# Optimization experiments

Measured on AMD Instinct MI355X. Metric: run time of the kernel, lower is better.

## Reference

```python
import jax, jax.numpy as jnp
import numpy as np


def _lstm_layer(xs, Wih, Whh, bih, bhh):
    # xs: [B, T, D_in]; PyTorch gate order: i, f, g, o
    B = xs.shape[0]
    H = Whh.shape[1]
    b = bih + bhh

    def step(carry, xt):
        h, c = carry
        g = xt @ Wih.T + h @ Whh.T + b          # [B, 4H]
        i, f, gg, o = jnp.split(g, 4, axis=-1)
        c = jax.nn.sigmoid(f) * c + jax.nn.sigmoid(i) * jnp.tanh(gg)
        h = jax.nn.sigmoid(o) * jnp.tanh(c)
        return (h, c), h

    h0 = jnp.zeros((B, H), xs.dtype)
    _, hs = jax.lax.scan(step, (h0, h0), xs.transpose(1, 0, 2))
    return hs.transpose(1, 0, 2)                # [B, T, H]


def setup_inputs() -> dict:
    key = jax.random.key(0)
    B, T, K, H, OUT = 64, 512, 8, 256, 24       # K = input_size = n fc heads
    HID1, HID2 = 100, 128                       # SAGE hidden / out feats

    ks = jax.random.split(key, 24)

    def rn(k, shape, s=0.05):
        return jax.random.normal(k, shape, dtype=jnp.float32) * s

    return {
        "x": jax.random.normal(ks[0], (B, T, K), dtype=jnp.float32),
        # LSTM layer 0
        "Wih0": rn(ks[1], (4 * H, K)), "Whh0": rn(ks[2], (4 * H, H)),
        "bih0": rn(ks[3], (4 * H,)),   "bhh0": rn(ks[4], (4 * H,)),
        # LSTM layer 1
        "Wih1": rn(ks[5], (4 * H, H)), "Whh1": rn(ks[6], (4 * H, H)),
        "bih1": rn(ks[7], (4 * H,)),   "bhh1": rn(ks[8], (4 * H,)),
        # SAGEConv1: lin_l (aggregated, with bias) + lin_r (root)
        "Wl1": rn(ks[9], (HID1, H)), "Wr1": rn(ks[10], (HID1, H)), "b1": rn(ks[11], (HID1,)),
        # SAGEConv2
        "Wl2": rn(ks[12], (HID2, HID1)), "Wr2": rn(ks[13], (HID2, HID1)), "b2": rn(ks[14], (HID2,)),
        # K stacked fc heads: Linear(128,64) -> ReLU -> Linear(64,OUT)
        "Wfc1": rn(ks[15], (K, 64, HID2)), "bfc1": rn(ks[16], (K, 64)),
        "Wfc2": rn(ks[17], (K, OUT, 64)),  "bfc2": rn(ks[18], (K, OUT)),
    }


def reference(x, Wih0, Whh0, bih0, bhh0, Wih1, Whh1, bih1, bhh1,
              Wl1, Wr1, b1, Wl2, Wr2, b2, Wfc1, bfc1, Wfc2, bfc2):
    # 2-layer LSTM (eval mode, dropout inactive)
    h = _lstm_layer(x, Wih0, Whh0, bih0, bhh0)   # [B, T, H]
    h = _lstm_layer(h, Wih1, Whh1, bih1, bhh1)   # [B, T, H]

    # softmax(feat@feat.T) > 0 everywhere => complete graph incl. self-loops,
    # and edge_weight is unused by GraphSAGE.forward, so SAGEConv mean aggregation
    # reduces exactly to the mean over all T nodes per graph.
    m = h.mean(axis=1, keepdims=True)            # [B, 1, H]
    h1 = jax.nn.elu(m @ Wl1.T + b1 + h @ Wr1.T)  # [B, T, 100]
    m1 = h1.mean(axis=1, keepdims=True)
    h2 = m1 @ Wl2.T + b2 + h1 @ Wr2.T            # [B, T, 128]

    s = h2[:, -1, :]                             # [B, 128] (last node)

    z = jax.nn.relu(jnp.einsum('bd,kod->kbo', s, Wfc1) + bfc1[:, None, :])
    pred = jnp.einsum('kbo,kpo->kbp', z, Wfc2) + bfc2[:, None, :]
    return pred                                   # [K, B, output_size]
```

## Files before the change

### kernel.cpp

```cpp
#include <hip/hip_runtime.h>
#include <stdint.h>

typedef _Float16 f16;
typedef _Float16 h2 __attribute__((ext_vector_type(2)));
typedef float f4 __attribute__((ext_vector_type(4)));

union F4H { f4 v; h2 h[4]; f16 s[8]; };

__device__ __forceinline__ float fdot2(h2 a, h2 b, float c) {
    return __builtin_amdgcn_fdot2(a, b, c, false);
}

__device__ __forceinline__ void lbar() {
    __builtin_amdgcn_sched_barrier(0);
    asm volatile("s_waitcnt lgkmcnt(0)" ::: "memory");
    __builtin_amdgcn_s_barrier();
    __builtin_amdgcn_sched_barrier(0);
}

#define NB 64
#define NT 512
#define NH 256
#define NG 1024

static const size_t OFF_H0   = 0;
static const size_t OFF_X1   = 16777216;
static const size_t OFF_H1   = 83886080;
static const size_t OFF_PL0  = 100663296;
static const size_t OFF_PL1  = 101187584;
static const size_t OFF_WIH1 = 101711872;
static const size_t OFF_WX0  = 102236160;
static const size_t OFF_B0C  = 102252544;
static const size_t OFF_B1C  = 102256640;
static const size_t OFF_WR1  = 102260736;
static const size_t OFF_MM   = 102326272;
static const size_t OFF_M1S  = 102391808;
static const size_t OFF_HL   = 102424576;
static const size_t OFF_FLG  = OFF_HL;

__device__ __forceinline__ void packw(const float* src, f4* dst, int id)
{
    const int j = id >> 5;
    const int g = id & 31;
    const float* s = src + j * 256 + g * 8;
    F4H u;
    #pragma unroll
    for (int i = 0; i < 8; ++i) u.s[i] = (f16)s[i];
    dst[g * 1024 + j] = u.v;
}

__global__ void pack_all(const float* __restrict__ Whh0, const float* __restrict__ Whh1,
                         const float* __restrict__ Wih1, const float* __restrict__ wih0,
                         const float* __restrict__ bih0, const float* __restrict__ bhh0,
                         const float* __restrict__ bih1, const float* __restrict__ bhh1,
                         const float* __restrict__ wr1,
                         f4* __restrict__ pl0, f4* __restrict__ pl1, f4* __restrict__ wih1p,
                         float* __restrict__ b0c, float* __restrict__ b1c,
                         h2* __restrict__ wx0p, f4* __restrict__ wr1p)
{
    const int id = blockIdx.x * 256 + threadIdx.x;
    if (id < 32768) {
        packw(Whh0, pl0, id);
    } else if (id < 65536) {
        packw(Whh1, pl1, id - 32768);
    } else if (id < 98304) {
        packw(Wih1, wih1p, id - 65536);
    } else if (id < 99328) {
        const int j = id - 98304;
        b0c[j] = bih0[j] + bhh0[j];
    } else if (id < 100352) {
        const int j = id - 99328;
        b1c[j] = bih1[j] + bhh1[j];
    } else if (id < 104448) {
        const int q = id - 100352;
        const int p = q >> 10, j = q & 1023;
        h2 v; v[0] = (f16)wih0[j * 8 + 2 * p]; v[1] = (f16)wih0[j * 8 + 2 * p + 1];
        wx0p[p * 1024 + j] = v;
    } else {
        const int q = id - 104448;
        const int g = q >> 7, o = q & 127;
        F4H u;
        #pragma unroll
        for (int i = 0; i < 8; ++i)
            u.s[i] = (o < 100) ? (f16)wr1[o * 256 + g * 8 + i] : (f16)0.f;
        wr1p[g * 128 + o] = u.v;
    }
}

#define DOT8(wa_, wb_, hh_) { F4H wa_u; wa_u.v = (wa_); F4H wb_u; wb_u.v = (wb_); F4H hh_u; hh_u.v = (hh_); \
    a0  = fdot2(wa_u.h[0], hh_u.h[0], a0 ); a1  = fdot2(wb_u.h[0], hh_u.h[0], a1 ); \
    a0b = fdot2(wa_u.h[1], hh_u.h[1], a0b); a1b = fdot2(wb_u.h[1], hh_u.h[1], a1b); \
    a0  = fdot2(wa_u.h[2], hh_u.h[2], a0 ); a1  = fdot2(wb_u.h[2], hh_u.h[2], a1 ); \
    a0b = fdot2(wa_u.h[3], hh_u.h[3], a0b); a1b = fdot2(wb_u.h[3], hh_u.h[3], a1b); }

#define STREAM_PHASES(HV) \
    _Pragma("unroll") \
    for (int p = 0; p < 6; ++p) { \
        if ((p & 1) == 0) { \
            DOT8(pA0[0], pA1[0], (HV)[20 + 2 * p]); \
            DOT8(pA0[1], pA1[1], (HV)[21 + 2 * p]); \
            if (p < 4) { \
                pA0[0] = str[(2 * (p + 2))     * 1024 + j0]; \
                pA1[0] = str[(2 * (p + 2))     * 1024 + j1]; \
                pA0[1] = str[(2 * (p + 2) + 1) * 1024 + j0]; \
                pA1[1] = str[(2 * (p + 2) + 1) * 1024 + j1]; \
            } \
        } else { \
            DOT8(pB0[0], pB1[0], (HV)[20 + 2 * p]); \
            DOT8(pB0[1], pB1[1], (HV)[21 + 2 * p]); \
            if (p < 4) { \
                pB0[0] = str[(2 * (p + 2))     * 1024 + j0]; \
                pB1[0] = str[(2 * (p + 2))     * 1024 + j1]; \
                pB0[1] = str[(2 * (p + 2) + 1) * 1024 + j0]; \
                pB1[1] = str[(2 * (p + 2) + 1) * 1024 + j1]; \
            } \
        } \
        DOT8(wrA[2 * p], wrB[2 * p], (HV)[9 + 2 * p]); \
        if (p < 5) DOT8(wrA[2 * p + 1], wrB[2 * p + 1], (HV)[10 + 2 * p]); \
    }

__global__ __launch_bounds__(512, 2)
void mega(const float* __restrict__ x,
          const f4* __restrict__ pl0, const f4* __restrict__ pl1,
          const f4* __restrict__ wih1p,
          const float* __restrict__ b0c, const float* __restrict__ b1c,
          const h2* __restrict__ wx0p,
          f16* __restrict__ h0, f16* __restrict__ x1, f16* __restrict__ h1,
          float* __restrict__ mmean, unsigned int* __restrict__ flags)
{
    __shared__ f4 wlds[9 * 1024];
    __shared__ float gates[1024];
    __shared__ __align__(16) f16 hsh[256];
    __shared__ __align__(16) h2 xsh[512 * 4];

    const int t = threadIdx.x;
    const int bid = blockIdx.x;
    const int role = bid >> 6;
    const int b = bid & 63;
    const int j0 = t, j1 = t + 512;

    if (role == 0) {
        const f4* pack = pl0;
        #pragma unroll
        for (int i = 0; i < 18; ++i) wlds[t + 512 * i] = pack[t + 512 * i];
        f4 wrA[11], wrB[11];
        #pragma unroll
        for (int g = 0; g < 11; ++g) {
            wrA[g] = pack[(9 + g) * 1024 + j0];
            wrB[g] = pack[(9 + g) * 1024 + j1];
        }
        #pragma unroll
        for (int g = 0; g < 11; ++g)
            asm volatile("" : "+v"(wrA[g]), "+v"(wrB[g]));
        const f4* str = pack + 20 * 1024;

        const float bc0 = b0c[j0], bc1 = b0c[j1];
        h2 wxA[4], wxB[4];
        #pragma unroll
        for (int p = 0; p < 4; ++p) { wxA[p] = wx0p[p * 1024 + j0]; wxB[p] = wx0p[p * 1024 + j1]; }
        const float* xb = x + ((size_t)b * NT + t) * 8;
        #pragma unroll
        for (int p = 0; p < 4; ++p) {
            h2 v; v[0] = (f16)xb[2 * p]; v[1] = (f16)xb[2 * p + 1];
            xsh[t * 4 + p] = v;
        }
        if (t < 32) { f4 zz = {0.f, 0.f, 0.f, 0.f}; ((f4*)hsh)[t] = zz; }
        float cst = 0.f;
        __syncthreads();

        f16* houtb = h0 + (size_t)b * NT * NH;
        unsigned int* myfl = flags + b * 16;

        #pragma unroll 1
        for (int tt = 0; tt < NT; ++tt) {
            f4 pA0[2], pA1[2], pB0[2], pB1[2];
            #pragma unroll
            for (int g = 0; g < 2; ++g) { pA0[g] = str[g * 1024 + j0]; pA1[g] = str[g * 1024 + j1]; }
            float a0 = bc0, a1 = bc1, a0b = 0.f, a1b = 0.f;
            #pragma unroll
            for (int p = 0; p < 4; ++p) {
                h2 xv = xsh[tt * 4 + p];
                a0 = fdot2(wxA[p], xv, a0);
                a1 = fdot2(wxB[p], xv, a1);
            }
            #pragma unroll
            for (int g = 0; g < 2; ++g) { pB0[g] = str[(2 + g) * 1024 + j0]; pB1[g] = str[(2 + g) * 1024 + j1]; }

            const f4* hv4 = (const f4*)hsh;
            #pragma unroll
            for (int i = 0; i < 9; ++i) DOT8(wlds[i * 1024 + j0], wlds[i * 1024 + j1], hv4[i]);
            STREAM_PHASES(hv4)

            gates[j0] = a0 + a0b;
            gates[j1] = a1 + a1b;
            lbar();

            if (t < 256) {
                float gi = gates[t], gf = gates[t + 256], gg = gates[t + 512], go = gates[t + 768];
                float si = 1.f / (1.f + __expf(-gi));
                float sf = 1.f / (1.f + __expf(-gf));
                float so = 1.f / (1.f + __expf(-go));
                float tg = 1.f - 2.f / (__expf(2.f * gg) + 1.f);
                cst = sf * cst + si * tg;
                float th = 1.f - 2.f / (__expf(2.f * cst) + 1.f);
                float hvl = so * th;
                hsh[t] = (f16)hvl;
                houtb[(size_t)tt * NH + t] = (f16)hvl;
            }
            if (((tt + 1) & 15) == 0) {
                __syncthreads();
                if (t == 0)
                    __hip_atomic_store(myfl, (unsigned)(tt + 1),
                                       __ATOMIC_RELEASE, __HIP_MEMORY_SCOPE_AGENT);
            } else {
                lbar();
            }
        }
    } else if (role == 1) {
        const float bc0 = b1c[j0], bc1 = b1c[j1];
        const f16* h0b = h0 + (size_t)b * NT * NH;
        f16* x1b = x1 + (size_t)b * NT * NG;
        const unsigned int* pfl = flags + b * 16;
        unsigned int* myfl = flags + 1024 + b * 16;
        f16* hrows = (f16*)xsh;
        bool dead = false;

        #pragma unroll 1
        for (int c = 0; c < 32; ++c) {
            if (t < 64 && !dead) {
                unsigned int guard = 0;
                while (__hip_atomic_load(pfl, __ATOMIC_ACQUIRE, __HIP_MEMORY_SCOPE_AGENT)
                       < (unsigned)((c + 1) * 16)) {
                    __builtin_amdgcn_s_sleep(8);
                    if (++guard > (1u << 16)) { dead = true; break; }
                }
            }
            __syncthreads();
            {
                const int rr = t >> 5, cc = t & 31;
                ((f4*)hrows)[t] = ((const f4*)(h0b + (size_t)(c * 16 + rr) * NH))[cc];
            }
            __syncthreads();

            float acc0[16], acc1[16];
            #pragma unroll
            for (int r = 0; r < 16; ++r) { acc0[r] = bc0; acc1[r] = bc1; }

            f4 w0 = wih1p[j0], w1 = wih1p[j1];
            #pragma unroll 1
            for (int g = 0; g < 32; ++g) {
                f4 n0 = w0, n1 = w1;
                if (g < 31) { n0 = wih1p[(g + 1) * 1024 + j0]; n1 = wih1p[(g + 1) * 1024 + j1]; }
                F4H W0; W0.v = w0; F4H W1; W1.v = w1;
                #pragma unroll
                for (int r = 0; r < 16; ++r) {
                    F4H H; H.v = ((const f4*)hrows)[r * 32 + g];
                    acc0[r] = fdot2(W0.h[0], H.h[0], acc0[r]);
                    acc0[r] = fdot2(W0.h[1], H.h[1], acc0[r]);
                    acc0[r] = fdot2(W0.h[2], H.h[2], acc0[r]);
                    acc0[r] = fdot2(W0.h[3], H.h[3], acc0[r]);
                    acc1[r] = fdot2(W1.h[0], H.h[0], acc1[r]);
                    acc1[r] = fdot2(W1.h[1], H.h[1], acc1[r]);
                    acc1[r] = fdot2(W1.h[2], H.h[2], acc1[r]);
                    acc1[r] = fdot2(W1.h[3], H.h[3], acc1[r]);
                }
                w0 = n0; w1 = n1;
            }
            #pragma unroll
            for (int r = 0; r < 16; ++r) {
                x1b[(size_t)(c * 16 + r) * NG + j0] = (f16)acc0[r];
                x1b[(size_t)(c * 16 + r) * NG + j1] = (f16)acc1[r];
            }
            __syncthreads();
            if (t == 0) __hip_atomic_store(myfl, (unsigned)(c + 1),
                                           __ATOMIC_RELEASE, __HIP_MEMORY_SCOPE_AGENT);
        }
    } else {
        const f4* pack = pl1;
        #pragma unroll
        for (int i = 0; i < 18; ++i) wlds[t + 512 * i] = pack[t + 512 * i];
        f4 wrA[11], wrB[11];
        #pragma unroll
        for (int g = 0; g < 11; ++g) {
            wrA[g] = pack[(9 + g) * 1024 + j0];
            wrB[g] = pack[(9 + g) * 1024 + j1];
        }
        #pragma unroll
        for (int g = 0; g < 11; ++g)
            asm volatile("" : "+v"(wrA[g]), "+v"(wrB[g]));
        const f4* str = pack + 20 * 1024;

        if (t < 32) { f4 zz = {0.f, 0.f, 0.f, 0.f}; ((f4*)hsh)[t] = zz; }
        float cst = 0.f, hsum = 0.f;
        __syncthreads();
        const f16* x1b = x1 + (size_t)b * NT * NG;
        f16* houtb = h1 + (size_t)b * NT * NH;
        const unsigned int* pfl = flags + 1024 + b * 16;
        bool dead = false;

        #pragma unroll 1
        for (int tt = 0; tt < NT; ++tt) {
            if ((tt & 15) == 0) {
                if (t < 64 && !dead) {
                    unsigned int guard = 0;
                    while (__hip_atomic_load(pfl, __ATOMIC_ACQUIRE, __HIP_MEMORY_SCOPE_AGENT)
                           < (unsigned)((tt >> 4) + 1)) {
                        __builtin_amdgcn_s_sleep(8);
                        if (++guard > (1u << 16)) { dead = true; break; }
                    }
                }
                __syncthreads();
            }

            f4 pA0[2], pA1[2], pB0[2], pB1[2];
            #pragma unroll
            for (int g = 0; g < 2; ++g) { pA0[g] = str[g * 1024 + j0]; pA1[g] = str[g * 1024 + j1]; }
            #pragma unroll
            for (int g = 0; g < 2; ++g) { pB0[g] = str[(2 + g) * 1024 + j0]; pB1[g] = str[(2 + g) * 1024 + j1]; }

            const f16* xr = x1b + (size_t)tt * NG;
            float a0 = (float)xr[j0];
            float a1 = (float)xr[j1];
            float a0b = 0.f, a1b = 0.f;

            const f4* hv4 = (const f4*)hsh;
            #pragma unroll
            for (int i = 0; i < 9; ++i) DOT8(wlds[i * 1024 + j0], wlds[i * 1024 + j1], hv4[i]);
            STREAM_PHASES(hv4)

            gates[j0] = a0 + a0b;
            gates[j1] = a1 + a1b;
            lbar();

            if (t < 256) {
                float gi = gates[t], gf = gates[t + 256], gg = gates[t + 512], go = gates[t + 768];
                float si = 1.f / (1.f + __expf(-gi));
                float sf = 1.f / (1.f + __expf(-gf));
                float so = 1.f / (1.f + __expf(-go));
                float tg = 1.f - 2.f / (__expf(2.f * gg) + 1.f);
                cst = sf * cst + si * tg;
                float th = 1.f - 2.f / (__expf(2.f * cst) + 1.f);
                float hvl = so * th;
                hsh[t] = (f16)hvl;
                houtb[(size_t)tt * NH + t] = (f16)hvl;
                hsum += hvl;
            }
            lbar();
        }
        if (t < 256) mmean[b * NH + t] = hsum * (1.f / 512.f);
    }
}

__global__ __launch_bounds__(256)
void k4a(const f16* __restrict__ h1, const float* __restrict__ mmean,
         const float* __restrict__ Wl1, const float* __restrict__ b1,
         const f4* __restrict__ wr1p, float* __restrict__ m1sum,
         float* __restrict__ hh1last)
{
    __shared__ __align__(16) f16 ash[64 * 256];
    __shared__ float msh[256];
    __shared__ float mbase[128];
    __shared__ float red[256];
    const int l = threadIdx.x;
    const int b = blockIdx.x >> 3;
    const int ch = blockIdx.x & 7;

    const f4* src = (const f4*)(h1 + ((size_t)b * 512 + ch * 64) * 256);
    f4* dst = (f4*)ash;
    #pragma unroll
    for (int i = 0; i < 8; ++i) dst[l + 256 * i] = src[l + 256 * i];
    msh[l] = mmean[b * 256 + l];
    __syncthreads();

    if (l < 128) {
        float acc = 0.f;
        if (l < 100) {
            acc = b1[l];
            const float* wrow = Wl1 + l * 256;
            for (int j = 0; j < 256; ++j) acc += msh[j] * wrow[j];
        }
        mbase[l] = acc;
    }
    __syncthreads();

    const int o = l & 127;
    const int th = l >> 7;
    float sumloc = 0.f;
    float last = 0.f;
    #pragma unroll 1
    for (int it = 0; it < 32; ++it) {
        const int tloc = it * 2 + th;
        float acc = mbase[o];
        const f4* arow = (const f4*)(ash + tloc * 256);
        #pragma unroll
        for (int u = 0; u < 32; ++u) {
            F4H av; av.v = arow[u];
            F4H wv; wv.v = wr1p[u * 128 + o];
            #pragma unroll
            for (int p = 0; p < 4; ++p) acc = fdot2(av.h[p], wv.h[p], acc);
        }
        float e = acc > 0.f ? acc : (__expf(acc) - 1.f);
        sumloc += e;
        if (tloc == 63) last = e;
    }
    red[l] = sumloc;
    __syncthreads();
    if (l < 128) {
        float s = red[l] + red[l + 128];
        if (l < 100) atomicAdd(m1sum + b * 128 + l, s);
    }
    if (ch == 7 && th == 1) hh1last[b * 128 + o] = last;
}

__global__ __launch_bounds__(128)
void k4b(const float* __restrict__ m1sum, const float* __restrict__ hh1last,
         const float* __restrict__ Wl2, const float* __restrict__ Wr2,
         const float* __restrict__ b2,
         const float* __restrict__ Wfc1, const float* __restrict__ bfc1,
         const float* __restrict__ Wfc2, const float* __restrict__ bfc2,
         float* __restrict__ out)
{
    __shared__ float m1s[128];
    __shared__ float hl[128];
    __shared__ float s[128];
    __shared__ float zsh[512];
    const int b = blockIdx.x;
    const int l = threadIdx.x;

    m1s[l] = m1sum[b * 128 + l] * (1.f / 512.f);
    hl[l] = hh1last[b * 128 + l];
    __syncthreads();

    {
        float acc = b2[l];
        const float* wl2r = Wl2 + l * 100;
        const float* wr2r = Wr2 + l * 100;
        for (int j = 0; j < 100; ++j) acc += m1s[j] * wl2r[j] + hl[j] * wr2r[j];
        s[l] = acc;
    }
    __syncthreads();

    #pragma unroll 1
    for (int i = 0; i < 4; ++i) {
        const int idx = l + 128 * i;
        const int k = idx >> 6, o = idx & 63;
        const float* w = Wfc1 + (size_t)(k * 64 + o) * 128;
        float a = bfc1[k * 64 + o];
        for (int d = 0; d < 128; ++d) a += s[d] * w[d];
        zsh[idx] = a > 0.f ? a : 0.f;
    }
    __syncthreads();

    #pragma unroll 1
    for (int i = 0; i < 2; ++i) {
        const int idx = l + 128 * i;
        if (idx < 192) {
            const int k = idx / 24, p = idx % 24;
            const float* w = Wfc2 + (size_t)(k * 24 + p) * 64;
            float a = bfc2[k * 24 + p];
            const float* z = zsh + k * 64;
            for (int d = 0; d < 64; ++d) a += z[d] * w[d];
            out[(size_t)(k * 64 + b) * 24 + p] = a;
        }
    }
}

extern "C" void kernel_launch(void* const* d_in, const int* in_sizes, int n_in,
                              void* d_out, int out_size, void* d_ws, size_t ws_size,
                              hipStream_t stream)
{
    const float* x    = (const float*)d_in[0];
    const float* Wih0 = (const float*)d_in[1];
    const float* Whh0 = (const float*)d_in[2];
    const float* bih0 = (const float*)d_in[3];
    const float* bhh0 = (const float*)d_in[4];
    const float* Wih1 = (const float*)d_in[5];
    const float* Whh1 = (const float*)d_in[6];
    const float* bih1 = (const float*)d_in[7];
    const float* bhh1 = (const float*)d_in[8];
    const float* Wl1  = (const float*)d_in[9];
    const float* Wr1  = (const float*)d_in[10];
    const float* b1   = (const float*)d_in[11];
    const float* Wl2  = (const float*)d_in[12];
    const float* Wr2  = (const float*)d_in[13];
    const float* b2   = (const float*)d_in[14];
    const float* Wfc1 = (const float*)d_in[15];
    const float* bfc1 = (const float*)d_in[16];
    const float* Wfc2 = (const float*)d_in[17];
    const float* bfc2 = (const float*)d_in[18];

    char* ws = (char*)d_ws;
    f16*   h0f   = (f16*)(ws + OFF_H0);
    f16*   x1f   = (f16*)(ws + OFF_X1);
    f16*   h1f   = (f16*)(ws + OFF_H1);
    f4*    pl0   = (f4*)(ws + OFF_PL0);
    f4*    pl1   = (f4*)(ws + OFF_PL1);
    f4*    wih1p = (f4*)(ws + OFF_WIH1);
    h2*    wx0p  = (h2*)(ws + OFF_WX0);
    float* b0c   = (float*)(ws + OFF_B0C);
    float* b1c   = (float*)(ws + OFF_B1C);
    f4*    wr1p  = (f4*)(ws + OFF_WR1);
    float* mm    = (float*)(ws + OFF_MM);
    float* m1s   = (float*)(ws + OFF_M1S);
    float* hhl   = (float*)(ws + OFF_HL);
    unsigned int* flg = (unsigned int*)(ws + OFF_FLG);

    pack_all<<<424, 256, 0, stream>>>(Whh0, Whh1, Wih1, Wih0,
                                      bih0, bhh0, bih1, bhh1, Wr1,
                                      pl0, pl1, wih1p, b0c, b1c, wx0p, wr1p);
    hipMemsetAsync(m1s, 0, 64 * 128 * sizeof(float), stream);
    hipMemsetAsync(flg, 0, 8192, stream);

    mega<<<192, 512, 0, stream>>>(x, pl0, pl1, wih1p, b0c, b1c, wx0p,
                                  h0f, x1f, h1f, mm, flg);

    k4a<<<512, 256, 0, stream>>>(h1f, mm, Wl1, b1, wr1p, m1s, hhl);
    k4b<<<64, 128, 0, stream>>>(m1s, hhl, Wl2, Wr2, b2, Wfc1, bfc1, Wfc2, bfc2, (float*)d_out);
}
```

Measured before the change: 1.256 ms.

## Permute gate columns so lane pairs hold all four gates, drop LDS gate exchange

The packed weights and biases are permuted so that each thread pair (t, t^1) computes the i,f,g,o gates for the same hidden unit. The gate pre-activations are then exchanged with a lane shuffle instead of being written to shared memory. This removes one block barrier per timestep, and the hidden state is double-buffered so the remaining barrier suffices. The cost is that every thread now evaluates the activation math, half of it redundantly, and the layout change depends on the pairing matching the pack order exactly.

```diff
diff --git a/kernel.cpp b/kernel.cpp
--- a/kernel.cpp
+++ b/kernel.cpp
@@ -38,11 +38,17 @@
 static const size_t OFF_HL   = 102424576;
 static const size_t OFF_FLG  = OFF_HL;
 
+__device__ __forceinline__ int permcol(int slot) {
+    const int s = slot & 511;
+    const int u = s >> 1, c = s & 1;
+    return (slot >> 9) * 512 + u + c * 256;
+}
+
 __device__ __forceinline__ void packw(const float* src, f4* dst, int id)
 {
     const int j = id >> 5;
     const int g = id & 31;
-    const float* s = src + j * 256 + g * 8;
+    const float* s = src + permcol(j) * 256 + g * 8;
     F4H u;
     #pragma unroll
     for (int i = 0; i < 8; ++i) u.s[i] = (f16)s[i];
@@ -67,14 +73,17 @@
         packw(Wih1, wih1p, id - 65536);
     } else if (id < 99328) {
         const int j = id - 98304;
-        b0c[j] = bih0[j] + bhh0[j];
+        const int pc = permcol(j);
+        b0c[j] = bih0[pc] + bhh0[pc];
     } else if (id < 100352) {
         const int j = id - 99328;
-        b1c[j] = bih1[j] + bhh1[j];
+        const int pc = permcol(j);
+        b1c[j] = bih1[pc] + bhh1[pc];
     } else if (id < 104448) {
         const int q = id - 100352;
         const int p = q >> 10, j = q & 1023;
-        h2 v; v[0] = (f16)wih0[j * 8 + 2 * p]; v[1] = (f16)wih0[j * 8 + 2 * p + 1];
+        const int pc = permcol(j);
+        h2 v; v[0] = (f16)wih0[pc * 8 + 2 * p]; v[1] = (f16)wih0[pc * 8 + 2 * p + 1];
         wx0p[p * 1024 + j] = v;
     } else {
         const int q = id - 104448;
@@ -129,8 +138,7 @@
           float* __restrict__ mmean, unsigned int* __restrict__ flags)
 {
     __shared__ f4 wlds[9 * 1024];
-    __shared__ float gates[1024];
-    __shared__ __align__(16) f16 hsh[256];
+    __shared__ __align__(16) f16 hbuf[2][256];
     __shared__ __align__(16) h2 xsh[512 * 4];
 
     const int t = threadIdx.x;
@@ -164,12 +172,13 @@
             h2 v; v[0] = (f16)xb[2 * p]; v[1] = (f16)xb[2 * p + 1];
             xsh[t * 4 + p] = v;
         }
-        if (t < 32) { f4 zz = {0.f, 0.f, 0.f, 0.f}; ((f4*)hsh)[t] = zz; }
+        if (t < 32) { f4 zz = {0.f, 0.f, 0.f, 0.f}; ((f4*)hbuf)[t] = zz; }
         float cst = 0.f;
         __syncthreads();
 
         f16* houtb = h0 + (size_t)b * NT * NH;
         unsigned int* myfl = flags + b * 16;
+        const int u = t >> 1, odd = t & 1;
 
         #pragma unroll 1
         for (int tt = 0; tt < NT; ++tt) {
@@ -186,26 +195,29 @@
             #pragma unroll
             for (int g = 0; g < 2; ++g) { pB0[g] = str[(2 + g) * 1024 + j0]; pB1[g] = str[(2 + g) * 1024 + j1]; }
 
-            const f4* hv4 = (const f4*)hsh;
+            const f4* hv4 = ((const f4*)hbuf) + (tt & 1) * 32;
             #pragma unroll
             for (int i = 0; i < 9; ++i) DOT8(wlds[i * 1024 + j0], wlds[i * 1024 + j1], hv4[i]);
             STREAM_PHASES(hv4)
 
-            gates[j0] = a0 + a0b;
-            gates[j1] = a1 + a1b;
-            lbar();
-
-            if (t < 256) {
-                float gi = gates[t], gf = gates[t + 256], gg = gates[t + 512], go = gates[t + 768];
-                float si = 1.f / (1.f + __expf(-gi));
-                float sf = 1.f / (1.f + __expf(-gf));
-                float so = 1.f / (1.f + __expf(-go));
-                float tg = 1.f - 2.f / (__expf(2.f * gg) + 1.f);
-                cst = sf * cst + si * tg;
-                float th = 1.f - 2.f / (__expf(2.f * cst) + 1.f);
-                float hvl = so * th;
-                hsh[t] = (f16)hvl;
-                houtb[(size_t)tt * NH + t] = (f16)hvl;
+            float av = a0 + a0b;
+            float bv = a1 + a1b;
+            float fa = __shfl_xor(av, 1, 64);
+            float fb = __shfl_xor(bv, 1, 64);
+            float gi = odd ? fa : av;
+            float gf = odd ? av : fa;
+            float gg = odd ? fb : bv;
+            float go = odd ? bv : fb;
+            float si = 1.f / (1.f + __expf(-gi));
+            float sf = 1.f / (1.f + __expf(-gf));
+            float so = 1.f / (1.f + __expf(-go));
+            float tg = 1.f - 2.f / (__expf(2.f * gg) + 1.f);
+            cst = sf * cst + si * tg;
+            float th = 1.f - 2.f / (__expf(2.f * cst) + 1.f);
+            float hvl = so * th;
+            if (!odd) {
+                hbuf[(tt & 1) ^ 1][u] = (f16)hvl;
+                houtb[(size_t)tt * NH + u] = (f16)hvl;
             }
             if (((tt + 1) & 15) == 0) {
                 __syncthreads();
@@ -290,13 +302,14 @@
             asm volatile("" : "+v"(wrA[g]), "+v"(wrB[g]));
         const f4* str = pack + 20 * 1024;
 
-        if (t < 32) { f4 zz = {0.f, 0.f, 0.f, 0.f}; ((f4*)hsh)[t] = zz; }
+        if (t < 32) { f4 zz = {0.f, 0.f, 0.f, 0.f}; ((f4*)hbuf)[t] = zz; }
         float cst = 0.f, hsum = 0.f;
         __syncthreads();
         const f16* x1b = x1 + (size_t)b * NT * NG;
         f16* houtb = h1 + (size_t)b * NT * NH;
         const unsigned int* pfl = flags + 1024 + b * 16;
         bool dead = false;
+        const int u = t >> 1, odd = t & 1;
 
         #pragma unroll 1
         for (int tt = 0; tt < NT; ++tt) {
@@ -323,31 +336,34 @@
             float a1 = (float)xr[j1];
             float a0b = 0.f, a1b = 0.f;
 
-            const f4* hv4 = (const f4*)hsh;
+            const f4* hv4 = ((const f4*)hbuf) + (tt & 1) * 32;
             #pragma unroll
             for (int i = 0; i < 9; ++i) DOT8(wlds[i * 1024 + j0], wlds[i * 1024 + j1], hv4[i]);
             STREAM_PHASES(hv4)
 
-            gates[j0] = a0 + a0b;
-            gates[j1] = a1 + a1b;
+            float av = a0 + a0b;
+            float bv = a1 + a1b;
+            float fa = __shfl_xor(av, 1, 64);
+            float fb = __shfl_xor(bv, 1, 64);
+            float gi = odd ? fa : av;
+            float gf = odd ? av : fa;
+            float gg = odd ? fb : bv;
+            float go = odd ? bv : fb;
+            float si = 1.f / (1.f + __expf(-gi));
+            float sf = 1.f / (1.f + __expf(-gf));
+            float so = 1.f / (1.f + __expf(-go));
+            float tg = 1.f - 2.f / (__expf(2.f * gg) + 1.f);
+            cst = sf * cst + si * tg;
+            float th = 1.f - 2.f / (__expf(2.f * cst) + 1.f);
+            float hvl = so * th;
+            if (!odd) {
+                hbuf[(tt & 1) ^ 1][u] = (f16)hvl;
+                houtb[(size_t)tt * NH + u] = (f16)hvl;
+                hsum += hvl;
+            }
             lbar();
-
-            if (t < 256) {
-                float gi = gates[t], gf = gates[t + 256], gg = gates[t + 512], go = gates[t + 768];
-                float si = 1.f / (1.f + __expf(-gi));
-                float sf = 1.f / (1.f + __expf(-gf));
-                float so = 1.f / (1.f + __expf(-go));
-                float tg = 1.f - 2.f / (__expf(2.f * gg) + 1.f);
-                cst = sf * cst + si * tg;
-                float th = 1.f - 2.f / (__expf(2.f * cst) + 1.f);
-                float hvl = so * th;
-                hsh[t] = (f16)hvl;
-                houtb[(size_t)tt * NH + t] = (f16)hvl;
-                hsum += hvl;
-            }
-            lbar();
-        }
-        if (t < 256) mmean[b * NH + t] = hsum * (1.f / 512.f);
+        }
+        if (!odd) mmean[b * NH + u] = hsum * (1.f / 512.f);
     }
 }
 
```

Result: faster. 1.220 ms (median of 2 runs) (-2.9%).
